# Kernel tuning notes

Measured on AMD Instinct MI355X. Metric: run time of the kernel, lower is better.

## Reference

```python
import jax, jax.numpy as jnp
import numpy as np


def setup_inputs() -> dict:
    key = jax.random.key(0)
    k_cb, k_mask, k_y, k_yt, k_ym = jax.random.split(key, 5)
    B, L, M = 8, 2048, 4096
    CB = jax.random.normal(k_cb, (B, L, 3), dtype=jnp.float32) * 10.0
    # residue validity mask: mostly valid, some padding
    mask = (jax.random.uniform(k_mask, (B, L)) > 0.1).astype(jnp.float32)
    Y = jax.random.normal(k_y, (B, M, 3), dtype=jnp.float32) * 10.0
    Y_t = jax.random.randint(k_yt, (B, M), 0, 64, dtype=jnp.int32)
    Y_m = jax.random.randint(k_ym, (B, M), 0, 2, dtype=jnp.int32)
    return {"CB": CB, "mask": mask, "Y": Y, "Y_t": Y_t, "Y_m": Y_m,
            "number_of_ligand_atoms": 25}


def reference(CB, mask, Y, Y_t, Y_m, number_of_ligand_atoms):
    # CB: [B, L, 3], mask: [B, L], Y: [B, M, 3], Y_t/Y_m: [B, M]
    B, L, _ = CB.shape
    k = number_of_ligand_atoms
    Y_m_f = Y_m.astype(jnp.float32)
    mask_CBY = mask[:, :, None] * Y_m_f[:, None, :]          # [B, L, M]
    d = CB[:, :, None, :] - Y[:, None, :, :]                 # [B, L, M, 3]
    L2_AB = jnp.sum(d * d, axis=-1)                          # [B, L, M]
    L2_AB = L2_AB * mask_CBY + (1.0 - mask_CBY) * 1000.0
    # k smallest distances per (b, l); torch uses full argsort + slice,
    # top_k of the negated matrix selects the same set.
    neg_vals, nn_idx = jax.lax.top_k(-L2_AB, k)              # [B, L, k]
    L2_AB_nn = -neg_vals
    D_AB_closest = jnp.sqrt(L2_AB_nn[:, :, 0])               # [B, L]
    b_idx = jnp.arange(B)[:, None, None]                     # [B, 1, 1]
    Y_out = Y[b_idx, nn_idx]                                 # [B, L, k, 3]
    Y_t_out = Y_t[b_idx, nn_idx].astype(jnp.int32)           # [B, L, k]
    Y_m_out = Y_m[b_idx, nn_idx].astype(jnp.int32)           # [B, L, k]
    return Y_out, Y_t_out, Y_m_out, D_AB_closest
```

## Files before the change

kernel.cpp:

```cpp
#include <hip/hip_runtime.h>

#pragma clang fp contract(off)

typedef unsigned long long u64;
typedef unsigned int u32;
typedef unsigned short u16;
typedef float f32x2 __attribute__((ext_vector_type(2)));

#define BB 8
#define LL 2048
#define MM 4096
#define KK 25
#define WPB 16
#define TPB 1024
#define CAP 3072
#define SENT  0xFFFFFFFFFFFFFFFFull
#define SENTH 0xFFFFFFFFu

static __device__ __forceinline__ u32 wave_min_u32(u32 x) {
    u32 t;
    t = (u32)__builtin_amdgcn_update_dpp(0, (int)x, 0xB1, 0xF, 0xF, true);
    x = t < x ? t : x;
    t = (u32)__builtin_amdgcn_update_dpp(0, (int)x, 0x4E, 0xF, 0xF, true);
    x = t < x ? t : x;
    t = (u32)__builtin_amdgcn_update_dpp(0, (int)x, 0x141, 0xF, 0xF, true);
    x = t < x ? t : x;
    t = (u32)__builtin_amdgcn_update_dpp(0, (int)x, 0x140, 0xF, 0xF, true);
    x = t < x ? t : x;
    t = (u32)__builtin_amdgcn_update_dpp((int)x, (int)x, 0x142, 0xF, 0xF, false);
    x = t < x ? t : x;
    t = (u32)__builtin_amdgcn_update_dpp((int)x, (int)x, 0x143, 0xF, 0xF, false);
    x = t < x ? t : x;
    return (u32)__builtin_amdgcn_readlane((int)x, 63);
}

__global__ void __launch_bounds__(TPB, 8) knn_kernel(
    const float* __restrict__ CB, const float* __restrict__ maskA,
    const float* __restrict__ Y, const int* __restrict__ Yt,
    const int* __restrict__ Ym, float* __restrict__ out)
{
    __shared__ __align__(16) float sX[CAP];
    __shared__ __align__(16) float sY[CAP];
    __shared__ __align__(16) float sZ[CAP];
    __shared__ u16 sT16[CAP];
    __shared__ u16 sMidx[64];
    __shared__ int sWinc[16];
    __shared__ int sWbase[16];
    __shared__ int sVtot;
    __shared__ u64 sExt[WPB][64];
    __shared__ u64 sR[WPB][KK];

    const int tid  = threadIdx.x;
    const int lane = tid & 63;
    const int wv   = tid >> 6;
    const int blk  = blockIdx.x;
    const int b    = blk >> 7;
    const int qg   = blk & 127;

    const float* Yb  = Y  + (size_t)b * MM * 3;
    const int*   Ymb = Ym + (size_t)b * MM;
    const int*   Ytb = Yt + (size_t)b * MM;

    const int p0 = tid << 2;
    const float4 f0 = *(const float4*)(Yb + 3 * p0);
    const float4 f1 = *(const float4*)(Yb + 3 * p0 + 4);
    const float4 f2 = *(const float4*)(Yb + 3 * p0 + 8);
    const int4   m4 = *(const int4*)(Ymb + p0);
    const int4   t4 = *(const int4*)(Ytb + p0);
    const int v0 = (m4.x != 0), v1 = (m4.y != 0), v2 = (m4.z != 0), v3 = (m4.w != 0);
    const int cnt0 = v0 + v1 + v2 + v3;

    int inc = cnt0;
#pragma unroll
    for (int off = 1; off < 64; off <<= 1) {
        const int t = __shfl_up(inc, off, 64);
        if (lane >= off) inc += t;
    }
    if (lane == 63) sWinc[wv] = inc;
    __syncthreads();
    if (tid < 16) {
        const int x = sWinc[tid];
        int ix = x;
#pragma unroll
        for (int off = 1; off < 16; off <<= 1) {
            const int t = __shfl_up(ix, off, 16);
            if (tid >= off) ix += t;
        }
        sWbase[tid] = ix - x;
        if (tid == 15) sVtot = ix;
    }
    __syncthreads();

    {
        int bs = sWbase[wv] + inc - cnt0;
        int mb = p0 - bs;
        if (v0) { sX[bs]=f0.x; sY[bs]=f0.y; sZ[bs]=f0.z; sT16[bs]=(u16)t4.x; bs++; }
        else    { if (mb < 64) sMidx[mb] = (u16)(p0 + 0); mb++; }
        if (v1) { sX[bs]=f0.w; sY[bs]=f1.x; sZ[bs]=f1.y; sT16[bs]=(u16)t4.y; bs++; }
        else    { if (mb < 64) sMidx[mb] = (u16)(p0 + 1); mb++; }
        if (v2) { sX[bs]=f1.z; sY[bs]=f1.w; sZ[bs]=f2.x; sT16[bs]=(u16)t4.z; bs++; }
        else    { if (mb < 64) sMidx[mb] = (u16)(p0 + 2); mb++; }
        if (v3) { sX[bs]=f2.y; sY[bs]=f2.z; sZ[bs]=f2.w; sT16[bs]=(u16)t4.w; bs++; }
        else    { if (mb < 64) sMidx[mb] = (u16)(p0 + 3); mb++; }
    }
    const int V  = sVtot;
    const int NJ = (V + 127) >> 7;
    for (int c = V + tid; c < (NJ << 7); c += TPB) {
        sX[c] = __builtin_inff(); sY[c] = 0.0f; sZ[c] = 0.0f; sT16[c] = 0;
    }
    __syncthreads();

    const int l = qg * WPB + wv;
    const int q = b * LL + l;

    float* out_y = out;
    float* out_t = out + (size_t)BB * LL * KK * 3;
    float* out_m = out_t + (size_t)BB * LL * KK;
    float* out_d = out_m + (size_t)BB * LL * KK;

    if (maskA[q] == 0.0f) {
        if (lane < KK) {
            const int p = lane;
            const size_t o = (size_t)q * KK + lane;
            out_y[3 * o + 0] = Yb[3 * p + 0];
            out_y[3 * o + 1] = Yb[3 * p + 1];
            out_y[3 * o + 2] = Yb[3 * p + 2];
            out_t[o] = (float)Ytb[p];
            out_m[o] = (float)Ymb[p];
            if (lane == 0) out_d[q] = sqrtf(1000.0f);
        }
        return;
    }

    const float cx = CB[3 * q + 0];
    const float cy = CB[3 * q + 1];
    const float cz = CB[3 * q + 2];

    float v1f = 3.0e38f, v2f = 3.0e38f, v3f = 3.0e38f, v4f = 3.0e38f;
    u32 J = 0u;
    const u32 SEL1 = 0x06050400u;
    const u32 SEL2 = 0x06050004u;
    const u32 SEL3 = 0x06000504u;
    const u32 SEL4 = 0x00060504u;
    auto ins = [&](float v, u32 id) {
        const bool c1 = v < v1f, c2 = v < v2f, c3 = v < v3f, c4 = v < v4f;
        const u32 sel = c1 ? SEL1 : (c2 ? SEL2 : (c3 ? SEL3 : SEL4));
        const u32 Jp  = __builtin_amdgcn_perm(J, id, sel);
        const float n2 = __builtin_amdgcn_fmed3f(v, v1f, v2f);
        const float n3 = __builtin_amdgcn_fmed3f(v, v2f, v3f);
        const float n4 = __builtin_amdgcn_fmed3f(v, v3f, v4f);
        v1f = fminf(v, v1f);
        v2f = n2; v3f = n3; v4f = n4;
        J = c4 ? Jp : J;
    };

    const f32x2 cxx = {cx, cx}, cyy = {cy, cy}, czz = {cz, cz};
#pragma unroll 4
    for (int j = 0; j < NJ; ++j) {
        const int base = (j << 7) + (lane << 1);
        const f32x2 xp = *(const f32x2*)&sX[base];
        const f32x2 yp = *(const f32x2*)&sY[base];
        const f32x2 zp = *(const f32x2*)&sZ[base];
        const f32x2 dx = cxx - xp;
        const f32x2 dy = cyy - yp;
        const f32x2 dz = czz - zp;
        const f32x2 dsq = (dx * dx + dy * dy) + dz * dz;
        ins(dsq.x, (u32)(j << 1));
        ins(dsq.y, (u32)((j << 1) | 1));
    }

    auto slotof = [&](u32 id) -> u32 {
        return ((id >> 1) << 7) | (u32)(lane << 1) | (id & 1u);
    };

    const u32 s1 = slotof( J        & 0xFFu);
    const u32 s2 = slotof((J >>  8) & 0xFFu);
    const u32 s3 = slotof((J >> 16) & 0xFFu);
    const u32 s4 = slotof((J >> 24) & 0xFFu);
    u32 h1 = __float_as_uint(v1f) + 1u;
    u32 h2 = __float_as_uint(v2f) + 1u;
    u32 h3 = __float_as_uint(v3f) + 1u;
    u32 h4 = __float_as_uint(v4f) + 1u;
    u64 lref = ((u64)h4 << 32) | s4;

    bool ladder = false;
    int  rstart = 0;
    {
        const u32 T = wave_min_u32(h4);
        const bool c1 = (h1 <= T), c2 = (h2 <= T), c3 = (h3 <= T), c4 = (h4 <= T);
        const u64 b1 = __ballot(c1), b2 = __ballot(c2);
        const u64 b3 = __ballot(c3), b4 = __ballot(c4);
        const int n1 = __popcll(b1), n2 = __popcll(b2), n3 = __popcll(b3);
        const int total = n1 + n2 + n3 + __popcll(b4);
        if (total > 64) {
            ladder = true;
        } else {
            const u64 below = (1ull << lane) - 1ull;
            u64* sE = sExt[wv];
            sE[lane] = SENT;
            if (lane == 24) sR[wv][24] = SENT;
            int pos = __popcll(b1 & below);
            if (c1) sE[pos] = ((u64)h1 << 32) | s1;
            pos = n1 + __popcll(b2 & below);
            if (c2) sE[pos] = ((u64)h2 << 32) | s2;
            pos = n1 + n2 + __popcll(b3 & below);
            if (c3) sE[pos] = ((u64)h3 << 32) | s3;
            pos = n1 + n2 + n3 + __popcll(b4 & below);
            if (c4) sE[pos] = ((u64)h4 << 32) | s4;
            const u64 mk = sE[lane];
            int rank = 0;
            const int tot = (total + 7) & ~7;
#pragma unroll 8
            for (int i = 0; i < tot; ++i)
                rank += (sE[i] < mk) ? 1 : 0;
            if (rank < KK && mk != SENT) sR[wv][rank] = mk;
            const u64 K25 = sR[wv][24];
            if (__any(lref < K25)) {
                const int scnt = (h1 < T) + (h2 < T) + (h3 < T) + (h4 < T);
                rstart = __popcll(__ballot(h1 < T)) + __popcll(__ballot(h2 < T))
                       + __popcll(__ballot(h3 < T)) + __popcll(__ballot(h4 < T));
#pragma unroll
                for (int k = 0; k < 4; ++k)
                    if (k < scnt) { h1 = h2; h2 = h3; h3 = h4; h4 = SENTH; J >>= 8; }
                ladder = true;
            }
        }
    }

    if (ladder) {
#pragma unroll 1
        for (int it = rstart; it < KK; ++it) {
            if (__any(h1 == SENTH)) {
                const bool need = (h1 == SENTH);
                u64 found = SENT;
                const int NI = NJ << 1;
#pragma unroll 4
                for (int id = 0; id < NI; ++id) {
                    const u32 s = slotof((u32)id);
                    const float dx = cx - sX[s];
                    const float dy = cy - sY[s];
                    const float dz = cz - sZ[s];
                    const float v = (dx * dx + dy * dy) + dz * dz;
                    const u64 key = ((u64)(__float_as_uint(v) + 1u) << 32) | s;
                    if (key > lref && key < found) found = key;
                }
                if (need) {
                    const u32 s = (u32)found & 0xFFFFu;
                    h1 = (u32)(found >> 32);
                    J = (J & ~0xFFu) | (((s >> 7) << 1) | (s & 1u));
                    lref = found;
                }
            }
            const u32 bv = wave_min_u32(h1);
            const u64 ball = __ballot(h1 == bv);
            bool win = (h1 == bv);
            if (__popcll(ball) != 1) {
                const u32 vl = slotof(J & 0xFFu);
                u32 cp = win ? vl : 0xFFFFFFFFu;
#pragma unroll
                for (int off = 32; off; off >>= 1) {
                    const u32 o = __shfl_xor(cp, off, 64);
                    cp = (o < cp) ? o : cp;
                }
                win = win && (vl == cp);
            }
            if (win) {
                sR[wv][it] = ((u64)h1 << 32) | slotof(J & 0xFFu);
                h1 = h2; h2 = h3; h3 = h4; h4 = SENTH;
                J >>= 8;
            }
        }
    }

    u64 myk = 0;
    if (lane < KK) myk = sR[wv][lane];
    const u32 mvh   = (u32)(myk >> 32);
    const u32 mslot = (u32)myk & 0xFFFFu;
    const bool less = (lane < KK) && (mvh < 0x447A0001u);
    const int nless = __popcll(__ballot(less));
    if (lane < KK) {
        const size_t o = (size_t)q * KK + lane;
        if (lane < nless) {
            out_y[3 * o + 0] = sX[mslot];
            out_y[3 * o + 1] = sY[mslot];
            out_y[3 * o + 2] = sZ[mslot];
            out_t[o] = (float)sT16[mslot];
            out_m[o] = 1.0f;
            if (lane == 0) out_d[q] = sqrtf(__uint_as_float(mvh - 1u));
        } else {
            const int p = (int)sMidx[lane - nless];
            out_y[3 * o + 0] = Yb[3 * p + 0];
            out_y[3 * o + 1] = Yb[3 * p + 1];
            out_y[3 * o + 2] = Yb[3 * p + 2];
            out_t[o] = (float)Ytb[p];
            out_m[o] = 0.0f;
            if (lane == 0) out_d[q] = sqrtf(1000.0f);
        }
    }
}

extern "C" void kernel_launch(void* const* d_in, const int* in_sizes, int n_in,
                              void* d_out, int out_size, void* d_ws, size_t ws_size,
                              hipStream_t stream) {
    const float* CB   = (const float*)d_in[0];
    const float* mask = (const float*)d_in[1];
    const float* Y    = (const float*)d_in[2];
    const int*   Yt   = (const int*)d_in[3];
    const int*   Ym   = (const int*)d_in[4];
    float* out = (float*)d_out;

    dim3 grid(BB * LL / WPB);
    dim3 block(TPB);
    hipLaunchKernelGGL(knn_kernel, grid, block, 0, stream, CB, mask, Y, Yt, Ym, out);
}
```

Before: 100.6 us.

## Process two query residues per wavefront to amortize LDS staging and loads

Each wavefront now handles two consecutive query points instead of one. The shared-memory ligand staging and the per-iteration LDS coordinate loads are shared across both queries, and the grid is halved. This cuts the per-block cost of compacting Y into LDS and the LDS read traffic per query. In exchange it raises register pressure from the doubled top-4 state, and the selection and ladder phases now run one after the other within each wave.

```diff
diff --git a/kernel.cpp b/kernel.cpp
--- a/kernel.cpp
+++ b/kernel.cpp
@@ -12,6 +12,7 @@
 #define MM 4096
 #define KK 25
 #define WPB 16
+#define QPW 2
 #define TPB 1024
 #define CAP 3072
 #define SENT  0xFFFFFFFFFFFFFFFFull
@@ -54,8 +55,8 @@
     const int lane = tid & 63;
     const int wv   = tid >> 6;
     const int blk  = blockIdx.x;
-    const int b    = blk >> 7;
-    const int qg   = blk & 127;
+    const int b    = blk >> 6;
+    const int qg   = blk & 63;
 
     const float* Yb  = Y  + (size_t)b * MM * 3;
     const int*   Ymb = Ym + (size_t)b * MM;
@@ -110,15 +111,16 @@
     }
     __syncthreads();
 
-    const int l = qg * WPB + wv;
-    const int q = b * LL + l;
+    const int lA = qg * (WPB * QPW) + (wv << 1);
+    const int qA = b * LL + lA;
+    const int qB = qA + 1;
 
     float* out_y = out;
     float* out_t = out + (size_t)BB * LL * KK * 3;
     float* out_m = out_t + (size_t)BB * LL * KK;
     float* out_d = out_m + (size_t)BB * LL * KK;
 
-    if (maskA[q] == 0.0f) {
+    auto fastout = [&](int q) {
         if (lane < KK) {
             const int p = lane;
             const size_t o = (size_t)q * KK + lane;
@@ -129,174 +131,195 @@
             out_m[o] = (float)Ymb[p];
             if (lane == 0) out_d[q] = sqrtf(1000.0f);
         }
-        return;
-    }
-
-    const float cx = CB[3 * q + 0];
-    const float cy = CB[3 * q + 1];
-    const float cz = CB[3 * q + 2];
-
-    float v1f = 3.0e38f, v2f = 3.0e38f, v3f = 3.0e38f, v4f = 3.0e38f;
-    u32 J = 0u;
+    };
+
+    const bool liveA = maskA[qA] != 0.0f;
+    const bool liveB = maskA[qB] != 0.0f;
+    if (!liveA) fastout(qA);
+    if (!liveB) fastout(qB);
+    if (!liveA && !liveB) return;
+
+    float cAx = CB[3 * qA + 0], cAy = CB[3 * qA + 1], cAz = CB[3 * qA + 2];
+    float cBx = CB[3 * qB + 0], cBy = CB[3 * qB + 1], cBz = CB[3 * qB + 2];
+    if (!liveA) { cAx = cBx; cAy = cBy; cAz = cBz; }
+    if (!liveB) { cBx = cAx; cBy = cAy; cBz = cAz; }
+
+    float vA1 = 3.0e38f, vA2 = 3.0e38f, vA3 = 3.0e38f, vA4 = 3.0e38f;
+    float vB1 = 3.0e38f, vB2 = 3.0e38f, vB3 = 3.0e38f, vB4 = 3.0e38f;
+    u32 JA = 0u, JB = 0u;
     const u32 SEL1 = 0x06050400u;
     const u32 SEL2 = 0x06050004u;
     const u32 SEL3 = 0x06000504u;
     const u32 SEL4 = 0x00060504u;
-    auto ins = [&](float v, u32 id) {
-        const bool c1 = v < v1f, c2 = v < v2f, c3 = v < v3f, c4 = v < v4f;
+    auto ins = [&](float v, u32 id, float& w1, float& w2, float& w3, float& w4,
+                   u32& JJ) {
+        const bool c1 = v < w1, c2 = v < w2, c3 = v < w3, c4 = v < w4;
         const u32 sel = c1 ? SEL1 : (c2 ? SEL2 : (c3 ? SEL3 : SEL4));
-        const u32 Jp  = __builtin_amdgcn_perm(J, id, sel);
-        const float n2 = __builtin_amdgcn_fmed3f(v, v1f, v2f);
-        const float n3 = __builtin_amdgcn_fmed3f(v, v2f, v3f);
-        const float n4 = __builtin_amdgcn_fmed3f(v, v3f, v4f);
-        v1f = fminf(v, v1f);
-        v2f = n2; v3f = n3; v4f = n4;
-        J = c4 ? Jp : J;
+        const u32 Jp  = __builtin_amdgcn_perm(JJ, id, sel);
+        const float n2 = __builtin_amdgcn_fmed3f(v, w1, w2);
+        const float n3 = __builtin_amdgcn_fmed3f(v, w2, w3);
+        const float n4 = __builtin_amdgcn_fmed3f(v, w3, w4);
+        w1 = fminf(v, w1);
+        w2 = n2; w3 = n3; w4 = n4;
+        JJ = c4 ? Jp : JJ;
     };
 
-    const f32x2 cxx = {cx, cx}, cyy = {cy, cy}, czz = {cz, cz};
+    const f32x2 cAxx = {cAx, cAx}, cAyy = {cAy, cAy}, cAzz = {cAz, cAz};
+    const f32x2 cBxx = {cBx, cBx}, cByy = {cBy, cBy}, cBzz = {cBz, cBz};
 #pragma unroll 4
     for (int j = 0; j < NJ; ++j) {
         const int base = (j << 7) + (lane << 1);
         const f32x2 xp = *(const f32x2*)&sX[base];
         const f32x2 yp = *(const f32x2*)&sY[base];
         const f32x2 zp = *(const f32x2*)&sZ[base];
-        const f32x2 dx = cxx - xp;
-        const f32x2 dy = cyy - yp;
-        const f32x2 dz = czz - zp;
-        const f32x2 dsq = (dx * dx + dy * dy) + dz * dz;
-        ins(dsq.x, (u32)(j << 1));
-        ins(dsq.y, (u32)((j << 1) | 1));
+        const f32x2 dxA = cAxx - xp;
+        const f32x2 dyA = cAyy - yp;
+        const f32x2 dzA = cAzz - zp;
+        const f32x2 dA = (dxA * dxA + dyA * dyA) + dzA * dzA;
+        const f32x2 dxB = cBxx - xp;
+        const f32x2 dyB = cByy - yp;
+        const f32x2 dzB = cBzz - zp;
+        const f32x2 dB = (dxB * dxB + dyB * dyB) + dzB * dzB;
+        ins(dA.x, (u32)(j << 1),       vA1, vA2, vA3, vA4, JA);
+        ins(dA.y, (u32)((j << 1) | 1), vA1, vA2, vA3, vA4, JA);
+        ins(dB.x, (u32)(j << 1),       vB1, vB2, vB3, vB4, JB);
+        ins(dB.y, (u32)((j << 1) | 1), vB1, vB2, vB3, vB4, JB);
     }
 
     auto slotof = [&](u32 id) -> u32 {
         return ((id >> 1) << 7) | (u32)(lane << 1) | (id & 1u);
     };
 
-    const u32 s1 = slotof( J        & 0xFFu);
-    const u32 s2 = slotof((J >>  8) & 0xFFu);
-    const u32 s3 = slotof((J >> 16) & 0xFFu);
-    const u32 s4 = slotof((J >> 24) & 0xFFu);
-    u32 h1 = __float_as_uint(v1f) + 1u;
-    u32 h2 = __float_as_uint(v2f) + 1u;
-    u32 h3 = __float_as_uint(v3f) + 1u;
-    u32 h4 = __float_as_uint(v4f) + 1u;
-    u64 lref = ((u64)h4 << 32) | s4;
-
-    bool ladder = false;
-    int  rstart = 0;
-    {
-        const u32 T = wave_min_u32(h4);
-        const bool c1 = (h1 <= T), c2 = (h2 <= T), c3 = (h3 <= T), c4 = (h4 <= T);
-        const u64 b1 = __ballot(c1), b2 = __ballot(c2);
-        const u64 b3 = __ballot(c3), b4 = __ballot(c4);
-        const int n1 = __popcll(b1), n2 = __popcll(b2), n3 = __popcll(b3);
-        const int total = n1 + n2 + n3 + __popcll(b4);
-        if (total > 64) {
-            ladder = true;
-        } else {
-            const u64 below = (1ull << lane) - 1ull;
-            u64* sE = sExt[wv];
-            sE[lane] = SENT;
-            if (lane == 24) sR[wv][24] = SENT;
-            int pos = __popcll(b1 & below);
-            if (c1) sE[pos] = ((u64)h1 << 32) | s1;
-            pos = n1 + __popcll(b2 & below);
-            if (c2) sE[pos] = ((u64)h2 << 32) | s2;
-            pos = n1 + n2 + __popcll(b3 & below);
-            if (c3) sE[pos] = ((u64)h3 << 32) | s3;
-            pos = n1 + n2 + n3 + __popcll(b4 & below);
-            if (c4) sE[pos] = ((u64)h4 << 32) | s4;
-            const u64 mk = sE[lane];
-            int rank = 0;
-            const int tot = (total + 7) & ~7;
+    auto process = [&](float v1f, float v2f, float v3f, float v4f, u32 J,
+                       float cx, float cy, float cz, int q) {
+        const u32 s1 = slotof( J        & 0xFFu);
+        const u32 s2 = slotof((J >>  8) & 0xFFu);
+        const u32 s3 = slotof((J >> 16) & 0xFFu);
+        const u32 s4 = slotof((J >> 24) & 0xFFu);
+        u32 h1 = __float_as_uint(v1f) + 1u;
+        u32 h2 = __float_as_uint(v2f) + 1u;
+        u32 h3 = __float_as_uint(v3f) + 1u;
+        u32 h4 = __float_as_uint(v4f) + 1u;
+        u64 lref = ((u64)h4 << 32) | s4;
+
+        bool ladder = false;
+        int  rstart = 0;
+        {
+            const u32 T = wave_min_u32(h4);
+            const bool c1 = (h1 <= T), c2 = (h2 <= T), c3 = (h3 <= T), c4 = (h4 <= T);
+            const u64 b1 = __ballot(c1), b2 = __ballot(c2);
+            const u64 b3 = __ballot(c3), b4 = __ballot(c4);
+            const int n1 = __popcll(b1), n2 = __popcll(b2), n3 = __popcll(b3);
+            const int total = n1 + n2 + n3 + __popcll(b4);
+            if (total > 64) {
+                ladder = true;
+            } else {
+                const u64 below = (1ull << lane) - 1ull;
+                u64* sE = sExt[wv];
+                sE[lane] = SENT;
+                if (lane == 24) sR[wv][24] = SENT;
+                int pos = __popcll(b1 & below);
+                if (c1) sE[pos] = ((u64)h1 << 32) | s1;
+                pos = n1 + __popcll(b2 & below);
+                if (c2) sE[pos] = ((u64)h2 << 32) | s2;
+                pos = n1 + n2 + __popcll(b3 & below);
+                if (c3) sE[pos] = ((u64)h3 << 32) | s3;
+                pos = n1 + n2 + n3 + __popcll(b4 & below);
+                if (c4) sE[pos] = ((u64)h4 << 32) | s4;
+                const u64 mk = sE[lane];
+                int rank = 0;
+                const int tot = (total + 7) & ~7;
 #pragma unroll 8
-            for (int i = 0; i < tot; ++i)
-                rank += (sE[i] < mk) ? 1 : 0;
-            if (rank < KK && mk != SENT) sR[wv][rank] = mk;
-            const u64 K25 = sR[wv][24];
-            if (__any(lref < K25)) {
-                const int scnt = (h1 < T) + (h2 < T) + (h3 < T) + (h4 < T);
-                rstart = __popcll(__ballot(h1 < T)) + __popcll(__ballot(h2 < T))
-                       + __popcll(__ballot(h3 < T)) + __popcll(__ballot(h4 < T));
+                for (int i = 0; i < tot; ++i)
+                    rank += (sE[i] < mk) ? 1 : 0;
+                if (rank < KK && mk != SENT) sR[wv][rank] = mk;
+                const u64 K25 = sR[wv][24];
+                if (__any(lref < K25)) {
+                    const int scnt = (h1 < T) + (h2 < T) + (h3 < T) + (h4 < T);
+                    rstart = __popcll(__ballot(h1 < T)) + __popcll(__ballot(h2 < T))
+                           + __popcll(__ballot(h3 < T)) + __popcll(__ballot(h4 < T));
 #pragma unroll
-                for (int k = 0; k < 4; ++k)
-                    if (k < scnt) { h1 = h2; h2 = h3; h3 = h4; h4 = SENTH; J >>= 8; }
-                ladder = true;
-            }
-        }
-    }
-
-    if (ladder) {
-#pragma unroll 1
-        for (int it = rstart; it < KK; ++it) {
-            if (__any(h1 == SENTH)) {
-                const bool need = (h1 == SENTH);
-                u64 found = SENT;
-                const int NI = NJ << 1;
-#pragma unroll 4
-                for (int id = 0; id < NI; ++id) {
-                    const u32 s = slotof((u32)id);
-                    const float dx = cx - sX[s];
-                    const float dy = cy - sY[s];
-                    const float dz = cz - sZ[s];
-                    const float v = (dx * dx + dy * dy) + dz * dz;
-                    const u64 key = ((u64)(__float_as_uint(v) + 1u) << 32) | s;
-                    if (key > lref && key < found) found = key;
-                }
-                if (need) {
-                    const u32 s = (u32)found & 0xFFFFu;
-                    h1 = (u32)(found >> 32);
-                    J = (J & ~0xFFu) | (((s >> 7) << 1) | (s & 1u));
-                    lref = found;
+                    for (int k = 0; k < 4; ++k)
+                        if (k < scnt) { h1 = h2; h2 = h3; h3 = h4; h4 = SENTH; J >>= 8; }
+                    ladder = true;
                 }
             }
-            const u32 bv = wave_min_u32(h1);
-            const u64 ball = __ballot(h1 == bv);
-            bool win = (h1 == bv);
-            if (__popcll(ball) != 1) {
-                const u32 vl = slotof(J & 0xFFu);
-                u32 cp = win ? vl : 0xFFFFFFFFu;
+        }
+
+        if (ladder) {
+#pragma unroll 1
+            for (int it = rstart; it < KK; ++it) {
+                if (__any(h1 == SENTH)) {
+                    const bool need = (h1 == SENTH);
+                    u64 found = SENT;
+                    const int NI = NJ << 1;
+#pragma unroll 4
+                    for (int id = 0; id < NI; ++id) {
+                        const u32 s = slotof((u32)id);
+                        const float dx = cx - sX[s];
+                        const float dy = cy - sY[s];
+                        const float dz = cz - sZ[s];
+                        const float v = (dx * dx + dy * dy) + dz * dz;
+                        const u64 key = ((u64)(__float_as_uint(v) + 1u) << 32) | s;
+                        if (key > lref && key < found) found = key;
+                    }
+                    if (need) {
+                        const u32 s = (u32)found & 0xFFFFu;
+                        h1 = (u32)(found >> 32);
+                        J = (J & ~0xFFu) | (((s >> 7) << 1) | (s & 1u));
+                        lref = found;
+                    }
+                }
+                const u32 bv = wave_min_u32(h1);
+                const u64 ball = __ballot(h1 == bv);
+                bool win = (h1 == bv);
+                if (__popcll(ball) != 1) {
+                    const u32 vl = slotof(J & 0xFFu);
+                    u32 cp = win ? vl : 0xFFFFFFFFu;
 #pragma unroll
-                for (int off = 32; off; off >>= 1) {
-                    const u32 o = __shfl_xor(cp, off, 64);
-                    cp = (o < cp) ? o : cp;
+                    for (int off = 32; off; off >>= 1) {
+                        const u32 o = __shfl_xor(cp, off, 64);
+                        cp = (o < cp) ? o : cp;
+                    }
+                    win = win && (vl == cp);
                 }
-                win = win && (vl == cp);
+                if (win) {
+                    sR[wv][it] = ((u64)h1 << 32) | slotof(J & 0xFFu);
+                    h1 = h2; h2 = h3; h3 = h4; h4 = SENTH;
+                    J >>= 8;
+                }
             }
-            if (win) {
-                sR[wv][it] = ((u64)h1 << 32) | slotof(J & 0xFFu);
-                h1 = h2; h2 = h3; h3 = h4; h4 = SENTH;
-                J >>= 8;
+        }
+
+        u64 myk = 0;
+        if (lane < KK) myk = sR[wv][lane];
+        const u32 mvh   = (u32)(myk >> 32);
+        const u32 mslot = (u32)myk & 0xFFFFu;
+        const bool less = (lane < KK) && (mvh < 0x447A0001u);
+        const int nless = __popcll(__ballot(less));
+        if (lane < KK) {
+            const size_t o = (size_t)q * KK + lane;
+            if (lane < nless) {
+                out_y[3 * o + 0] = sX[mslot];
+                out_y[3 * o + 1] = sY[mslot];
+                out_y[3 * o + 2] = sZ[mslot];
+                out_t[o] = (float)sT16[mslot];
+                out_m[o] = 1.0f;
+                if (lane == 0) out_d[q] = sqrtf(__uint_as_float(mvh - 1u));
+            } else {
+                const int p = (int)sMidx[lane - nless];
+                out_y[3 * o + 0] = Yb[3 * p + 0];
+                out_y[3 * o + 1] = Yb[3 * p + 1];
+                out_y[3 * o + 2] = Yb[3 * p + 2];
+                out_t[o] = (float)Ytb[p];
+                out_m[o] = 0.0f;
+                if (lane == 0) out_d[q] = sqrtf(1000.0f);
             }
         }
-    }
-
-    u64 myk = 0;
-    if (lane < KK) myk = sR[wv][lane];
-    const u32 mvh   = (u32)(myk >> 32);
-    const u32 mslot = (u32)myk & 0xFFFFu;
-    const bool less = (lane < KK) && (mvh < 0x447A0001u);
-    const int nless = __popcll(__ballot(less));
-    if (lane < KK) {
-        const size_t o = (size_t)q * KK + lane;
-        if (lane < nless) {
-            out_y[3 * o + 0] = sX[mslot];
-            out_y[3 * o + 1] = sY[mslot];
-            out_y[3 * o + 2] = sZ[mslot];
-            out_t[o] = (float)sT16[mslot];
-            out_m[o] = 1.0f;
-            if (lane == 0) out_d[q] = sqrtf(__uint_as_float(mvh - 1u));
-        } else {
-            const int p = (int)sMidx[lane - nless];
-            out_y[3 * o + 0] = Yb[3 * p + 0];
-            out_y[3 * o + 1] = Yb[3 * p + 1];
-            out_y[3 * o + 2] = Yb[3 * p + 2];
-            out_t[o] = (float)Ytb[p];
-            out_m[o] = 0.0f;
-            if (lane == 0) out_d[q] = sqrtf(1000.0f);
-        }
-    }
+    };
+
+    if (liveA) process(vA1, vA2, vA3, vA4, JA, cAx, cAy, cAz, qA);
+    if (liveB) process(vB1, vB2, vB3, vB4, JB, cBx, cBy, cBz, qB);
 }
 
 extern "C" void kernel_launch(void* const* d_in, const int* in_sizes, int n_in,
@@ -309,7 +332,7 @@
     const int*   Ym   = (const int*)d_in[4];
     float* out = (float*)d_out;
 
-    dim3 grid(BB * LL / WPB);
+    dim3 grid(BB * LL / (WPB * QPW));
     dim3 block(TPB);
     hipLaunchKernelGGL(knn_kernel, grid, block, 0, stream, CB, mask, Y, Yt, Ym, out);
 }
```

Measured after the change: 114.2 us. 1.13x slower.

## Threshold-filter all candidates using cached 16-bit distance prefixes instead of per-lane index tracking

Applied to the files above, without the earlier changes.

Replaces per-lane top-4 index tracking (perm-based slot packing) with a value-only top-4 pass that also caches the high 16 bits of every distance in registers. A wave-wide threshold is then applied across all candidates, recomputing exact distances only for those whose prefix passes, and compacting them into shared memory for rank-based selection. The loop bound is fixed at a compile-time 18 chunks so the loop fully unrolls. The fallback ladder is reworked to use 64-bit keys with a full rescan excluding already-collected candidates. This removes the perm/select work from the hot loop and the frequent fallback to the ladder, at the cost of more registers and always scanning 18 chunks even when fewer valid atoms exist.

```diff
diff --git a/kernel.cpp b/kernel.cpp
--- a/kernel.cpp
+++ b/kernel.cpp
@@ -14,8 +14,9 @@
 #define WPB 16
 #define TPB 1024
 #define CAP 3072
+#define NJF 18
+#define NSLOT (NJF << 7)
 #define SENT  0xFFFFFFFFFFFFFFFFull
-#define SENTH 0xFFFFFFFFu
 
 static __device__ __forceinline__ u32 wave_min_u32(u32 x) {
     u32 t;
@@ -47,7 +48,7 @@
     __shared__ int sWinc[16];
     __shared__ int sWbase[16];
     __shared__ int sVtot;
-    __shared__ u64 sExt[WPB][64];
+    __shared__ __align__(16) u64 sExt[WPB][64];
     __shared__ u64 sR[WPB][KK];
 
     const int tid  = threadIdx.x;
@@ -103,9 +104,8 @@
         if (v3) { sX[bs]=f2.y; sY[bs]=f2.z; sZ[bs]=f2.w; sT16[bs]=(u16)t4.w; bs++; }
         else    { if (mb < 64) sMidx[mb] = (u16)(p0 + 3); mb++; }
     }
-    const int V  = sVtot;
-    const int NJ = (V + 127) >> 7;
-    for (int c = V + tid; c < (NJ << 7); c += TPB) {
+    const int V = sVtot;
+    for (int c = V + tid; c < NSLOT; c += TPB) {
         sX[c] = __builtin_inff(); sY[c] = 0.0f; sZ[c] = 0.0f; sT16[c] = 0;
     }
     __syncthreads();
@@ -137,26 +137,18 @@
     const float cz = CB[3 * q + 2];
 
     float v1f = 3.0e38f, v2f = 3.0e38f, v3f = 3.0e38f, v4f = 3.0e38f;
-    u32 J = 0u;
-    const u32 SEL1 = 0x06050400u;
-    const u32 SEL2 = 0x06050004u;
-    const u32 SEL3 = 0x06000504u;
-    const u32 SEL4 = 0x00060504u;
-    auto ins = [&](float v, u32 id) {
-        const bool c1 = v < v1f, c2 = v < v2f, c3 = v < v3f, c4 = v < v4f;
-        const u32 sel = c1 ? SEL1 : (c2 ? SEL2 : (c3 ? SEL3 : SEL4));
-        const u32 Jp  = __builtin_amdgcn_perm(J, id, sel);
+    u32 d16[NJF];
+    auto insv = [&](float v) {
         const float n2 = __builtin_amdgcn_fmed3f(v, v1f, v2f);
         const float n3 = __builtin_amdgcn_fmed3f(v, v2f, v3f);
         const float n4 = __builtin_amdgcn_fmed3f(v, v3f, v4f);
         v1f = fminf(v, v1f);
         v2f = n2; v3f = n3; v4f = n4;
-        J = c4 ? Jp : J;
     };
 
     const f32x2 cxx = {cx, cx}, cyy = {cy, cy}, czz = {cz, cz};
-#pragma unroll 4
-    for (int j = 0; j < NJ; ++j) {
+#pragma unroll
+    for (int j = 0; j < NJF; ++j) {
         const int base = (j << 7) + (lane << 1);
         const f32x2 xp = *(const f32x2*)&sX[base];
         const f32x2 yp = *(const f32x2*)&sY[base];
@@ -165,97 +157,128 @@
         const f32x2 dy = cyy - yp;
         const f32x2 dz = czz - zp;
         const f32x2 dsq = (dx * dx + dy * dy) + dz * dz;
-        ins(dsq.x, (u32)(j << 1));
-        ins(dsq.y, (u32)((j << 1) | 1));
-    }
-
-    auto slotof = [&](u32 id) -> u32 {
-        return ((id >> 1) << 7) | (u32)(lane << 1) | (id & 1u);
-    };
-
-    const u32 s1 = slotof( J        & 0xFFu);
-    const u32 s2 = slotof((J >>  8) & 0xFFu);
-    const u32 s3 = slotof((J >> 16) & 0xFFu);
-    const u32 s4 = slotof((J >> 24) & 0xFFu);
-    u32 h1 = __float_as_uint(v1f) + 1u;
-    u32 h2 = __float_as_uint(v2f) + 1u;
-    u32 h3 = __float_as_uint(v3f) + 1u;
-    u32 h4 = __float_as_uint(v4f) + 1u;
-    u64 lref = ((u64)h4 << 32) | s4;
-
-    bool ladder = false;
+        d16[j] = __builtin_amdgcn_perm(__float_as_uint(dsq.y),
+                                       __float_as_uint(dsq.x), 0x07060302u);
+        insv(dsq.x);
+        insv(dsq.y);
+    }
+
+    const u32 Tw  = wave_min_u32(__float_as_uint(v4f));
+    const u32 T16 = Tw >> 16;
+    const u64 below = (1ull << lane) - 1ull;
+    u64* sE = sExt[wv];
+    sE[lane] = SENT;
+
+    int  total = 0;
+    bool overflow = false;
+#pragma unroll
+    for (int j = 0; j < NJF; ++j) {
+        const u32 pk = d16[j];
+        bool c0 = (pk & 0xFFFFu) <= T16;
+        bool c1 = (pk >> 16)     <= T16;
+        const int sl0 = (j << 7) | (lane << 1);
+        u32 bv0 = 0, bv1 = 0;
+        if (c0) {
+            const float dx = cx - sX[sl0];
+            const float dy = cy - sY[sl0];
+            const float dz = cz - sZ[sl0];
+            bv0 = __float_as_uint((dx * dx + dy * dy) + dz * dz);
+            c0 = (bv0 <= Tw);
+        }
+        if (c1) {
+            const float dx = cx - sX[sl0 + 1];
+            const float dy = cy - sY[sl0 + 1];
+            const float dz = cz - sZ[sl0 + 1];
+            bv1 = __float_as_uint((dx * dx + dy * dy) + dz * dz);
+            c1 = (bv1 <= Tw);
+        }
+        const u64 b0 = __ballot(c0), b1 = __ballot(c1);
+        const int n0 = __popcll(b0);
+        const int nt = n0 + __popcll(b1);
+        if (total + nt > 64) { overflow = true; break; }
+        if (c0) sE[total + __popcll(b0 & below)] =
+                    ((u64)(bv0 + 1u) << 32) | (u32)sl0;
+        if (c1) sE[total + n0 + __popcll(b1 & below)] =
+                    ((u64)(bv1 + 1u) << 32) | (u32)(sl0 | 1);
+        total += nt;
+    }
+
+    bool fire = overflow;
     int  rstart = 0;
-    {
-        const u32 T = wave_min_u32(h4);
-        const bool c1 = (h1 <= T), c2 = (h2 <= T), c3 = (h3 <= T), c4 = (h4 <= T);
-        const u64 b1 = __ballot(c1), b2 = __ballot(c2);
-        const u64 b3 = __ballot(c3), b4 = __ballot(c4);
-        const int n1 = __popcll(b1), n2 = __popcll(b2), n3 = __popcll(b3);
-        const int total = n1 + n2 + n3 + __popcll(b4);
-        if (total > 64) {
-            ladder = true;
-        } else {
-            const u64 below = (1ull << lane) - 1ull;
-            u64* sE = sExt[wv];
-            sE[lane] = SENT;
-            if (lane == 24) sR[wv][24] = SENT;
-            int pos = __popcll(b1 & below);
-            if (c1) sE[pos] = ((u64)h1 << 32) | s1;
-            pos = n1 + __popcll(b2 & below);
-            if (c2) sE[pos] = ((u64)h2 << 32) | s2;
-            pos = n1 + n2 + __popcll(b3 & below);
-            if (c3) sE[pos] = ((u64)h3 << 32) | s3;
-            pos = n1 + n2 + n3 + __popcll(b4 & below);
-            if (c4) sE[pos] = ((u64)h4 << 32) | s4;
-            const u64 mk = sE[lane];
-            int rank = 0;
-            const int tot = (total + 7) & ~7;
+    if (!overflow) {
+        const u64 mk = sE[lane];
+        int rank = 0;
+        const int tot = (total + 7) & ~7;
 #pragma unroll 8
-            for (int i = 0; i < tot; ++i)
-                rank += (sE[i] < mk) ? 1 : 0;
-            if (rank < KK && mk != SENT) sR[wv][rank] = mk;
-            const u64 K25 = sR[wv][24];
-            if (__any(lref < K25)) {
-                const int scnt = (h1 < T) + (h2 < T) + (h3 < T) + (h4 < T);
-                rstart = __popcll(__ballot(h1 < T)) + __popcll(__ballot(h2 < T))
-                       + __popcll(__ballot(h3 < T)) + __popcll(__ballot(h4 < T));
-#pragma unroll
-                for (int k = 0; k < 4; ++k)
-                    if (k < scnt) { h1 = h2; h2 = h3; h3 = h4; h4 = SENTH; J >>= 8; }
-                ladder = true;
+        for (int i = 0; i < tot; ++i)
+            rank += (sE[i] < mk) ? 1 : 0;
+        if (mk != SENT && rank < KK) sR[wv][rank] = mk;
+        if (total < KK) { fire = true; rstart = total; }
+    }
+
+    if (fire) {
+        u64 k1 = SENT, k2 = SENT, k3 = SENT, k4 = SENT;
+#pragma unroll 2
+        for (int j = 0; j < NJF; ++j) {
+            const int base = (j << 7) + (lane << 1);
+            const f32x2 xp = *(const f32x2*)&sX[base];
+            const f32x2 yp = *(const f32x2*)&sY[base];
+            const f32x2 zp = *(const f32x2*)&sZ[base];
+            const f32x2 dx = cxx - xp;
+            const f32x2 dy = cyy - yp;
+            const f32x2 dz = czz - zp;
+            const f32x2 dsq = (dx * dx + dy * dy) + dz * dz;
+#pragma unroll
+            for (int h = 0; h < 2; ++h) {
+                const u32 bv = __float_as_uint(h ? dsq.y : dsq.x);
+                const bool incl = overflow || (bv > Tw);
+                const u64 key = incl
+                    ? (((u64)(bv + 1u) << 32) | (u32)(base + h)) : SENT;
+                const bool c1 = key < k1, c2 = key < k2,
+                           c3 = key < k3, c4 = key < k4;
+                const u64 n4 = c4 ? (c3 ? k3 : key) : k4;
+                const u64 n3 = c3 ? (c2 ? k2 : key) : k3;
+                const u64 n2 = c2 ? (c1 ? k1 : key) : k2;
+                k1 = c1 ? key : k1;
+                k2 = n2; k3 = n3; k4 = n4;
             }
         }
-    }
-
-    if (ladder) {
+        u64 lref = k4;
 #pragma unroll 1
         for (int it = rstart; it < KK; ++it) {
-            if (__any(h1 == SENTH)) {
-                const bool need = (h1 == SENTH);
+            if (__any(k1 == SENT)) {
+                const bool need = (k1 == SENT);
                 u64 found = SENT;
-                const int NI = NJ << 1;
-#pragma unroll 4
-                for (int id = 0; id < NI; ++id) {
-                    const u32 s = slotof((u32)id);
-                    const float dx = cx - sX[s];
-                    const float dy = cy - sY[s];
-                    const float dz = cz - sZ[s];
-                    const float v = (dx * dx + dy * dy) + dz * dz;
-                    const u64 key = ((u64)(__float_as_uint(v) + 1u) << 32) | s;
-                    if (key > lref && key < found) found = key;
+                if (need) {
+#pragma unroll 2
+                    for (int j = 0; j < NJF; ++j) {
+                        const int base = (j << 7) + (lane << 1);
+                        const f32x2 xp = *(const f32x2*)&sX[base];
+                        const f32x2 yp = *(const f32x2*)&sY[base];
+                        const f32x2 zp = *(const f32x2*)&sZ[base];
+                        const f32x2 dx = cxx - xp;
+                        const f32x2 dy = cyy - yp;
+                        const f32x2 dz = czz - zp;
+                        const f32x2 dsq = (dx * dx + dy * dy) + dz * dz;
+#pragma unroll
+                        for (int h = 0; h < 2; ++h) {
+                            const u32 bv = __float_as_uint(h ? dsq.y : dsq.x);
+                            const bool incl = overflow || (bv > Tw);
+                            const u64 key = incl
+                                ? (((u64)(bv + 1u) << 32) | (u32)(base + h))
+                                : SENT;
+                            if (key > lref && key < found) found = key;
+                        }
+                    }
                 }
-                if (need) {
-                    const u32 s = (u32)found & 0xFFFFu;
-                    h1 = (u32)(found >> 32);
-                    J = (J & ~0xFFu) | (((s >> 7) << 1) | (s & 1u));
-                    lref = found;
-                }
+                if (need) { k1 = found; if (found != SENT) lref = found; }
             }
-            const u32 bv = wave_min_u32(h1);
-            const u64 ball = __ballot(h1 == bv);
-            bool win = (h1 == bv);
+            const u32 vh = (u32)(k1 >> 32);
+            const u32 bv = wave_min_u32(vh);
+            const u64 ball = __ballot(vh == bv);
+            bool win = (vh == bv);
             if (__popcll(ball) != 1) {
-                const u32 vl = slotof(J & 0xFFu);
+                const u32 vl = (u32)k1;
                 u32 cp = win ? vl : 0xFFFFFFFFu;
 #pragma unroll
                 for (int off = 32; off; off >>= 1) {
@@ -265,9 +288,8 @@
                 win = win && (vl == cp);
             }
             if (win) {
-                sR[wv][it] = ((u64)h1 << 32) | slotof(J & 0xFFu);
-                h1 = h2; h2 = h3; h3 = h4; h4 = SENTH;
-                J >>= 8;
+                sR[wv][it] = k1;
+                k1 = k2; k2 = k3; k3 = k4; k4 = SENT;
             }
         }
     }
```

Result: slower. 146.0 us (+45.1%).
